# Kernel optimization log

Measured on AMD Instinct MI355X. Metric: run time of the kernel, lower is better.

## Reference

```python
import jax, jax.numpy as jnp
import numpy as np

N = 50000
E = 800000
DIM = 128          # dim_drug = atom_embedding_dim
N_ATOM_TYPES = 44
N_FIXED = 34


def setup_inputs() -> dict:
    key = jax.random.key(0)
    ks = jax.random.split(key, 9)
    x = jax.random.normal(ks[0], (N, N_ATOM_TYPES + N_FIXED), dtype=jnp.float32)
    edge_index = jax.random.randint(ks[1], (2, E), 0, N, dtype=jnp.int64)
    batch = jax.random.randint(ks[2], (N,), 0, 512, dtype=jnp.int64)
    s = 1.0 / np.sqrt(DIM)
    emb = jax.random.normal(ks[3], (N_ATOM_TYPES, DIM), dtype=jnp.float32)
    lin_W = jax.random.normal(ks[4], (DIM, DIM + N_FIXED), dtype=jnp.float32) * s
    lin_b = jnp.zeros((DIM,), dtype=jnp.float32)
    gcn1_W = jax.random.normal(ks[5], (DIM, DIM), dtype=jnp.float32) * s
    gcn1_b = jnp.zeros((DIM,), dtype=jnp.float32)
    gcn2_W = jax.random.normal(ks[6], (DIM, DIM), dtype=jnp.float32) * s
    gcn2_b = jnp.zeros((DIM,), dtype=jnp.float32)
    return {"x": x, "edge_index": edge_index, "batch": batch,
            "emb": emb, "lin_W": lin_W, "lin_b": lin_b,
            "gcn1_W": gcn1_W, "gcn1_b": gcn1_b,
            "gcn2_W": gcn2_W, "gcn2_b": gcn2_b}


def _gcn_conv(h, src, dst, norm, W, b, n):
    # PyG GCNConv: linear (no bias) -> normalized gather/scatter-add -> + bias
    h = h @ W.T                                    # [N, D]
    msg = h[src] * norm[:, None]                   # gather + scale, [E+N, D]
    out = jax.ops.segment_sum(msg, dst, num_segments=n)  # scatter-add
    return out + b


def reference(x, edge_index, batch, emb, lin_W, lin_b,
              gcn1_W, gcn1_b, gcn2_W, gcn2_b):
    n = x.shape[0]
    # embedding of argmax over one-hot atom-type block
    idx = jnp.argmax(x[:, :N_ATOM_TYPES], axis=1)
    h = jnp.concatenate([emb[idx], x[:, N_ATOM_TYPES:]], axis=1)  # [N, D+34]
    h = jax.nn.relu(h @ lin_W.T + lin_b)  # dropout = identity (eval)

    # GCN normalization with self-loops, shared by both layers
    loops = jnp.arange(n, dtype=edge_index.dtype)
    src = jnp.concatenate([edge_index[0], loops])
    dst = jnp.concatenate([edge_index[1], loops])
    deg = jax.ops.segment_sum(jnp.ones_like(dst, dtype=h.dtype), dst, num_segments=n)
    dinv = jnp.where(deg > 0, jax.lax.rsqrt(deg), 0.0)
    norm = dinv[src] * dinv[dst]                   # [E+N]

    h = jax.nn.relu(_gcn_conv(h, src, dst, norm, gcn1_W, gcn1_b, n))
    h = jax.nn.relu(_gcn_conv(h, src, dst, norm, gcn2_W, gcn2_b, n))
    return h
```

## Files before the change

### kernel.cpp

```cpp
#include <hip/hip_runtime.h>

#define NFEAT 78
#define NTYPES 44
#define NFIX 34
#define DIM 128
#define LIN_K 162
#define FIXP 36
#define APAD 132
#define TILE 32
#define RPAD 64
#define BSH 5
#define NSUB 64
#define SCAP 32

typedef unsigned int uint32;
typedef unsigned short ushort_t;

__device__ __forceinline__ uint32 ctr_decode(uint32 c) {
    uint32 p = c - 0xAAAAAAAAu;
    return (p < 1024u) ? p : c;
}

__device__ __forceinline__ unsigned short f2bf(float f) {
    uint32 u = __float_as_uint(f);
    u += 0x7FFFu + ((u >> 16) & 1u);
    return (unsigned short)(u >> 16);
}
__device__ __forceinline__ void bf_acc(uint4 v, float4& A, float4& B) {
    A.x += __uint_as_float(v.x << 16); A.y += __uint_as_float(v.x & 0xFFFF0000u);
    A.z += __uint_as_float(v.y << 16); A.w += __uint_as_float(v.y & 0xFFFF0000u);
    B.x += __uint_as_float(v.z << 16); B.y += __uint_as_float(v.z & 0xFFFF0000u);
    B.z += __uint_as_float(v.w << 16); B.w += __uint_as_float(v.w & 0xFFFF0000u);
}

__device__ __forceinline__ void agg_row(
    const ushort_t* __restrict__ row, const uint4* __restrict__ h4,
    long t, int l, int len, int NM1, float4& A, float4& B)
{
    bf_acc(h4[t * 16 + l], A, B);
    int nct = (len + 7) >> 3;
    if (nct <= 0) return;
    const uint4* row4 = (const uint4*)row;

#define MG1(D, S) { int _s = (int)(S); if (_s > NM1) _s = NM1; D = h4[(long)_s * 16 + l]; }
#define GATH8(P, I) \
    MG1(P##0, (I).x & 0xFFFFu) MG1(P##1, (I).x >> 16) \
    MG1(P##2, (I).y & 0xFFFFu) MG1(P##3, (I).y >> 16) \
    MG1(P##4, (I).z & 0xFFFFu) MG1(P##5, (I).z >> 16) \
    MG1(P##6, (I).w & 0xFFFFu) MG1(P##7, (I).w >> 16)
#define ACC8(P) \
    { bf_acc(P##0, A, B); bf_acc(P##1, A, B); bf_acc(P##2, A, B); bf_acc(P##3, A, B); \
      bf_acc(P##4, A, B); bf_acc(P##5, A, B); bf_acc(P##6, A, B); bf_acc(P##7, A, B); }
#define MACC8(P, kb) \
    { if ((kb) + 0 < len) bf_acc(P##0, A, B); \
      if ((kb) + 1 < len) bf_acc(P##1, A, B); \
      if ((kb) + 2 < len) bf_acc(P##2, A, B); \
      if ((kb) + 3 < len) bf_acc(P##3, A, B); \
      if ((kb) + 4 < len) bf_acc(P##4, A, B); \
      if ((kb) + 5 < len) bf_acc(P##5, A, B); \
      if ((kb) + 6 < len) bf_acc(P##6, A, B); \
      if ((kb) + 7 < len) bf_acc(P##7, A, B); }

    uint4 va0, va1, va2, va3, va4, va5, va6, va7;
    uint4 vb0, vb1, vb2, vb3, vb4, vb5, vb6, vb7;
    uint4 I0   = row4[0];
    uint4 Inxt = row4[1];
    GATH8(va, I0);
    int c = 1;
    for (; c + 1 < nct; c += 2) {
        uint4 Ib  = Inxt;
        uint4 In1 = row4[c + 1];
        GATH8(vb, Ib);
        int c2 = c + 2; if (c2 > 7) c2 = 7;
        uint4 In2 = row4[c2];
        ACC8(va);
        GATH8(va, In1);
        ACC8(vb);
        Inxt = In2;
    }
    if (c < nct) {
        GATH8(vb, Inxt);
        ACC8(va);
        MACC8(vb, c << 3);
    } else {
        MACC8(va, (c - 1) << 3);
    }
#undef MG1
#undef GATH8
#undef ACC8
#undef MACC8
}

__global__ __launch_bounds__(256) void k_prep(
    const int* __restrict__ esrc, const int* __restrict__ edst,
    uint32* __restrict__ bcur, uint32* __restrict__ brec, int E, int nbE, int NB,
    const float* __restrict__ w0, const float* __restrict__ w1,
    const float* __restrict__ w2, const float* __restrict__ emb,
    const float* __restrict__ lin_b,
    float* __restrict__ t0, float* __restrict__ t1, float* __restrict__ t2,
    float* __restrict__ embWb)
{
    __shared__ float smem[32 * 33];
    const int bid = blockIdx.x;
    const int tid = threadIdx.x;
    if (bid < nbE) {
        int e = bid * 256 + tid;
        if (e < E) {
            int d = edst[e], s = esrc[e];
            int sb = (bid & 63) * NB + (d >> BSH);
            uint32 old = atomicAdd(&bcur[sb], 1u);
            uint32 pos = ctr_decode(old);
            if (pos < SCAP)
                brec[(size_t)sb * SCAP + pos] = (uint32)s | ((uint32)(d & 31) << 16);
        }
        return;
    }
    if (bid < nbE + 72) {
        int bb = bid - nbE;
        int sel = bb / 24, b = bb % 24;
        const float* src = sel == 0 ? w0 : (sel == 1 ? w1 : w2);
        float*       dst = sel == 0 ? t0 : (sel == 1 ? t1 : t2);
        const int C = (sel == 0) ? LIN_K : DIM;
        int tc = (C + 31) / 32;
        int bx = b % tc, by = b / tc;
        if (by >= 4) return;
        float (*tile)[33] = (float(*)[33])smem;
        int ty = tid >> 5, tx = tid & 31;
        int c0 = bx * 32, r0 = by * 32;
        #pragma unroll
        for (int j = 0; j < 32; j += 8) {
            int r = r0 + ty + j, c = c0 + tx;
            tile[ty + j][tx] = (r < 128 && c < C) ? src[r * C + c] : 0.0f;
        }
        __syncthreads();
        #pragma unroll
        for (int j = 0; j < 32; j += 8) {
            int c = c0 + ty + j, r = r0 + tx;
            if (c < C) dst[c * 128 + r] = tile[tx][ty + j];
        }
        return;
    }
    int t = bid - nbE - 72;
    if (tid < DIM) smem[tid] = emb[t * DIM + tid];
    __syncthreads();
    if (tid < DIM) {
        float acc = lin_b[tid];
        const float* wr = w0 + (long)tid * LIN_K;
        #pragma unroll 4
        for (int k = 0; k < DIM; ++k)
            acc = fmaf(smem[k], wr[k], acc);
        embWb[t * DIM + tid] = acc;
    }
}

__global__ __launch_bounds__(256) void k_binembed(
    const uint32* __restrict__ bcur, const uint32* __restrict__ brec,
    uint32* __restrict__ cursor, ushort_t* __restrict__ csr,
    const float* __restrict__ x, const float* __restrict__ embWb,
    const float* __restrict__ W2t, const float* __restrict__ Wt,
    unsigned short* __restrict__ hs1, int N, int NB)
{
    __shared__ ushort_t lcsr[32][RPAD];
    __shared__ uint32   lcnt[32];
    __shared__ uint32   scnt[NSUB];
    __shared__ float    s_x[TILE][80];
    __shared__ int      s_idx[TILE];
    __shared__ float    s_h[TILE][APAD];
    const int b     = blockIdx.x;
    const int tid   = threadIdx.x;
    const int node0 = b * 32;

    if (tid < 32) lcnt[tid] = 0;
    if (tid < NSUB) {
        uint32 c = ctr_decode(bcur[(size_t)tid * NB + b]);
        scnt[tid] = (c < SCAP) ? c : SCAP;
    }
    {
        uint32* p = (uint32*)lcsr;
        for (int i = tid; i < 32 * RPAD / 2; i += 256) p[i] = 0xAAAAAAAAu;
    }
    __syncthreads();
    {
        const int sub = tid >> 2, r0 = tid & 3;
        uint32 cnt = scnt[sub];
        const uint32* rec = brec + ((size_t)sub * NB + b) * SCAP;
        for (uint32 r = r0; r < cnt; r += 4) {
            uint32 v = rec[r];
            int dloc = (int)(v >> 16);
            uint32 pos = atomicAdd(&lcnt[dloc], 1u);
            if (pos < RPAD) lcsr[dloc][pos] = (ushort_t)(v & 0xFFFFu);
        }
    }
    {
        const float* xb = x + (size_t)node0 * NFEAT;
        int nv = N - node0; if (nv > TILE) nv = TILE;
        int limit = nv * NFEAT;
        int nf4 = limit >> 2;
        for (int f4 = tid; f4 < nf4; f4 += 256) {
            float4 v = *(const float4*)(xb + 4 * f4);
            int f = 4 * f4;
            { int m = f / NFEAT, c = f - m * NFEAT;                s_x[m][c] = v.x; }
            { int g = f + 1; int m = g / NFEAT, c = g - m * NFEAT; s_x[m][c] = v.y; }
            { int g = f + 2; int m = g / NFEAT, c = g - m * NFEAT; s_x[m][c] = v.z; }
            { int g = f + 3; int m = g / NFEAT, c = g - m * NFEAT; s_x[m][c] = v.w; }
        }
        for (int f = (nf4 << 2) + tid; f < limit; f += 256) {
            int m = f / NFEAT, c = f - m * NFEAT;
            s_x[m][c] = xb[f];
        }
        if (nv < TILE) {
            for (int q = tid; q < (TILE - nv) * NFEAT; q += 256) {
                int m = nv + q / NFEAT, c = q % NFEAT;
                s_x[m][c] = 0.0f;
            }
        }
    }
    __syncthreads();
    {
        const uint4* src = (const uint4*)lcsr;
        uint4* dst = (uint4*)(csr + (size_t)node0 * RPAD);
        int row = tid >> 3;
        if (node0 + row < N) dst[tid] = src[tid];
        if (tid < 32 && node0 + tid < N) cursor[node0 + tid] = lcnt[tid];
    }
    if (tid < TILE) {
        int bi = 0;
        if (node0 + tid < N) {
            float best = s_x[tid][0];
            for (int k = 1; k < NTYPES; ++k) {
                float v = s_x[tid][k];
                if (v > best) { best = v; bi = k; }
            }
        }
        s_idx[tid] = bi;
    }
    __syncthreads();

    const int tx = tid & 31;
    const int m0 = (tid >> 5) * 4;
    const float4* W2t4 = (const float4*)W2t;
    const float4* eb4  = (const float4*)embWb;
    float4 acc[4];
    #pragma unroll
    for (int j = 0; j < 4; ++j) acc[j] = eb4[s_idx[m0 + j] * 32 + tx];
    for (int k = 0; k < 32; k += 8) {
        float4 w[8];
        #pragma unroll
        for (int u = 0; u < 8; ++u) w[u] = W2t4[(k + u) * 32 + tx];
        #pragma unroll
        for (int u = 0; u < 8; ++u) {
            #pragma unroll
            for (int j = 0; j < 4; ++j) {
                float a = s_x[m0 + j][NTYPES + k + u];
                acc[j].x = fmaf(a, w[u].x, acc[j].x);
                acc[j].y = fmaf(a, w[u].y, acc[j].y);
                acc[j].z = fmaf(a, w[u].z, acc[j].z);
                acc[j].w = fmaf(a, w[u].w, acc[j].w);
            }
        }
    }
    {
        float4 w0 = W2t4[32 * 32 + tx];
        float4 w1 = W2t4[33 * 32 + tx];
        #pragma unroll
        for (int j = 0; j < 4; ++j) {
            float a0 = s_x[m0 + j][NTYPES + 32], a1 = s_x[m0 + j][NTYPES + 33];
            acc[j].x = fmaf(a1, w1.x, fmaf(a0, w0.x, acc[j].x));
            acc[j].y = fmaf(a1, w1.y, fmaf(a0, w0.y, acc[j].y));
            acc[j].z = fmaf(a1, w1.z, fmaf(a0, w0.z, acc[j].z));
            acc[j].w = fmaf(a1, w1.w, fmaf(a0, w0.w, acc[j].w));
        }
    }
    #pragma unroll
    for (int j = 0; j < 4; ++j) {
        float4 o;
        o.x = fmaxf(acc[j].x, 0.0f); o.y = fmaxf(acc[j].y, 0.0f);
        o.z = fmaxf(acc[j].z, 0.0f); o.w = fmaxf(acc[j].w, 0.0f);
        *((float4*)&s_h[m0 + j][4 * tx]) = o;
    }
    __syncthreads();

    const float4* Wt4 = (const float4*)Wt;
    float4 c[4];
    #pragma unroll
    for (int j = 0; j < 4; ++j) c[j] = make_float4(0, 0, 0, 0);
    for (int k = 0; k < DIM; k += 8) {
        float4 w[8];
        #pragma unroll
        for (int u = 0; u < 8; ++u) w[u] = Wt4[(k + u) * 32 + tx];
        #pragma unroll
        for (int u = 0; u < 8; ++u) {
            #pragma unroll
            for (int j = 0; j < 4; ++j) {
                float a = s_h[m0 + j][k + u];
                c[j].x = fmaf(a, w[u].x, c[j].x);
                c[j].y = fmaf(a, w[u].y, c[j].y);
                c[j].z = fmaf(a, w[u].z, c[j].z);
                c[j].w = fmaf(a, w[u].w, c[j].w);
            }
        }
    }
    #pragma unroll
    for (int j = 0; j < 4; ++j) {
        int n = node0 + m0 + j;
        if (n < N) {
            float di = rsqrtf((float)(lcnt[m0 + j] + 1u));
            ushort4 o;
            o.x = f2bf(c[j].x * di); o.y = f2bf(c[j].y * di);
            o.z = f2bf(c[j].z * di); o.w = f2bf(c[j].w * di);
            ((ushort4*)hs1)[(long)n * 32 + tx] = o;
        }
    }
}

__global__ __launch_bounds__(256) void k_agg_gemm2(
    const ushort_t* __restrict__ csr, const uint32* __restrict__ cursor,
    const unsigned short* __restrict__ hs1, const float* __restrict__ b1,
    const float* __restrict__ Wt, unsigned short* __restrict__ hs2, int N)
{
    __shared__ float s_a[TILE][APAD];
    const int tid = threadIdx.x;
    const int node0 = blockIdx.x * TILE;
    const int qw = tid >> 4, l = tid & 15;
    const uint4* h4 = (const uint4*)hs1;
    const float4* b4 = (const float4*)b1;
    float4 bb0 = b4[2 * l], bb1 = b4[2 * l + 1];

    #pragma unroll
    for (int p = 0; p < 2; ++p) {
        int m = qw * 2 + p;
        int t = node0 + m;
        float4 A = make_float4(0, 0, 0, 0), B = make_float4(0, 0, 0, 0);
        if (t < N) {
            uint32 deg = ctr_decode(cursor[t]);
            int len = (deg < RPAD) ? (int)deg : RPAD;
            agg_row(csr + (size_t)t * RPAD, h4, (long)t, l, len, N - 1, A, B);
            float dt = rsqrtf((float)(deg + 1u));
            A.x = fmaxf(fmaf(A.x, dt, bb0.x), 0.0f);
            A.y = fmaxf(fmaf(A.y, dt, bb0.y), 0.0f);
            A.z = fmaxf(fmaf(A.z, dt, bb0.z), 0.0f);
            A.w = fmaxf(fmaf(A.w, dt, bb0.w), 0.0f);
            B.x = fmaxf(fmaf(B.x, dt, bb1.x), 0.0f);
            B.y = fmaxf(fmaf(B.y, dt, bb1.y), 0.0f);
            B.z = fmaxf(fmaf(B.z, dt, bb1.z), 0.0f);
            B.w = fmaxf(fmaf(B.w, dt, bb1.w), 0.0f);
        }
        *((float4*)&s_a[m][8 * l])     = A;
        *((float4*)&s_a[m][8 * l + 4]) = B;
    }
    __syncthreads();

    const int tx = tid & 31;
    const int m0 = (tid >> 5) * 4;
    const float4* Wt4 = (const float4*)Wt;
    float4 c[4];
    #pragma unroll
    for (int j = 0; j < 4; ++j) c[j] = make_float4(0, 0, 0, 0);
    for (int k = 0; k < DIM; k += 8) {
        float4 w[8];
        #pragma unroll
        for (int u = 0; u < 8; ++u) w[u] = Wt4[(k + u) * 32 + tx];
        #pragma unroll
        for (int u = 0; u < 8; ++u) {
            #pragma unroll
            for (int j = 0; j < 4; ++j) {
                float a = s_a[m0 + j][k + u];
                c[j].x = fmaf(a, w[u].x, c[j].x);
                c[j].y = fmaf(a, w[u].y, c[j].y);
                c[j].z = fmaf(a, w[u].z, c[j].z);
                c[j].w = fmaf(a, w[u].w, c[j].w);
            }
        }
    }
    #pragma unroll
    for (int j = 0; j < 4; ++j) {
        int n = node0 + m0 + j;
        if (n < N) {
            float di = rsqrtf((float)(ctr_decode(cursor[n]) + 1u));
            ushort4 o;
            o.x = f2bf(c[j].x * di); o.y = f2bf(c[j].y * di);
            o.z = f2bf(c[j].z * di); o.w = f2bf(c[j].w * di);
            ((ushort4*)hs2)[(long)n * 32 + tx] = o;
        }
    }
}

__global__ __launch_bounds__(256) void k_agg_out(
    const ushort_t* __restrict__ csr, const uint32* __restrict__ cursor,
    const unsigned short* __restrict__ hs2, const float* __restrict__ b2,
    float* __restrict__ out, int N)
{
    int t = blockIdx.x * 16 + (threadIdx.x >> 4);
    int l = threadIdx.x & 15;
    if (t >= N) return;
    const uint4* h4 = (const uint4*)hs2;
    const float4* b4 = (const float4*)b2;
    float4 bb0 = b4[2 * l], bb1 = b4[2 * l + 1];
    float4 A = make_float4(0, 0, 0, 0), B = make_float4(0, 0, 0, 0);
    uint32 deg = ctr_decode(cursor[t]);
    int len = (deg < RPAD) ? (int)deg : RPAD;
    agg_row(csr + (size_t)t * RPAD, h4, (long)t, l, len, N - 1, A, B);
    float dt = rsqrtf((float)(deg + 1u));
    float4 o0, o1;
    o0.x = fmaxf(fmaf(A.x, dt, bb0.x), 0.0f);
    o0.y = fmaxf(fmaf(A.y, dt, bb0.y), 0.0f);
    o0.z = fmaxf(fmaf(A.z, dt, bb0.z), 0.0f);
    o0.w = fmaxf(fmaf(A.w, dt, bb0.w), 0.0f);
    o1.x = fmaxf(fmaf(B.x, dt, bb1.x), 0.0f);
    o1.y = fmaxf(fmaf(B.y, dt, bb1.y), 0.0f);
    o1.z = fmaxf(fmaf(B.z, dt, bb1.z), 0.0f);
    o1.w = fmaxf(fmaf(B.w, dt, bb1.w), 0.0f);
    ((float4*)out)[(long)t * 32 + 2 * l]     = o0;
    ((float4*)out)[(long)t * 32 + 2 * l + 1] = o1;
}

extern "C" void kernel_launch(void* const* d_in, const int* in_sizes, int n_in,
                              void* d_out, int out_size, void* d_ws, size_t ws_size,
                              hipStream_t stream) {
    const float* x     = (const float*)d_in[0];
    const int*   edge  = (const int*)d_in[1];
    const float* emb   = (const float*)d_in[3];
    const float* lin_W = (const float*)d_in[4];
    const float* lin_b = (const float*)d_in[5];
    const float* g1W   = (const float*)d_in[6];
    const float* g1b   = (const float*)d_in[7];
    const float* g2W   = (const float*)d_in[8];
    const float* g2b   = (const float*)d_in[9];
    float* out = (float*)d_out;

    const int N = in_sizes[0] / NFEAT;
    const int E = in_sizes[1] / 2;
    const int* esrc = edge;
    const int* edst = edge + E;
    const int NB = (N + 31) / 32;

    uint32* cursor = (uint32*)d_ws;
    ushort_t* csr  = (ushort_t*)(cursor + N);
    uint32* bcur   = (uint32*)(csr + (size_t)N * RPAD);
    uint32* brec   = bcur + (size_t)NB * NSUB;
    float* linWt   = (float*)(brec + (size_t)NB * NSUB * SCAP);
    float* g1Wt    = linWt + LIN_K * DIM;
    float* g2Wt    = g1Wt + DIM * DIM;
    float* embWb   = g2Wt + DIM * DIM;
    unsigned short* hs1 = (unsigned short*)(embWb + NTYPES * DIM);
    unsigned short* hs2 = hs1 + (size_t)N * DIM;

    const int nbE  = (E + 255) / 256;
    const int nb32 = (N + TILE - 1) / TILE;
    const int nbC  = (N + 15) / 16;

    k_prep<<<nbE + 72 + NTYPES, 256, 0, stream>>>(
        esrc, edst, bcur, brec, E, nbE, NB,
        lin_W, g1W, g2W, emb, lin_b, linWt, g1Wt, g2Wt, embWb);
    k_binembed<<<NB, 256, 0, stream>>>(
        bcur, brec, cursor, csr, x, embWb, linWt + DIM * DIM, g1Wt, hs1, N, NB);
    k_agg_gemm2<<<nb32, 256, 0, stream>>>(csr, cursor, hs1, g1b, g2Wt, hs2, N);
    k_agg_out<<<nbC, 256, 0, stream>>>(csr, cursor, hs2, g2b, out, N);
}
```

Baseline: 261.4 us.

## Use split-bf16 MFMA for both GCN weight GEMMs

Replaces the scalar FP32 FMA loops for the two 128x128 GCN weight multiplies with MFMA 16x16x32 bf16 instructions. Each operand is split into hi and lo bf16 parts, and three MFMAs per tile keep accuracy close to FP32. The weights are pre-split and pre-swizzled into MFMA fragment layout in the prep kernel, and the per-row degree normalisation is cached in shared memory. The cost is extra conversion work on activations and lower-precision arithmetic, and the output stores become scattered 2-byte writes.

```diff
diff --git a/kernel.cpp b/kernel.cpp
--- a/kernel.cpp
+++ b/kernel.cpp
@@ -5,7 +5,6 @@
 #define NFIX 34
 #define DIM 128
 #define LIN_K 162
-#define FIXP 36
 #define APAD 132
 #define TILE 32
 #define RPAD 64
@@ -15,6 +14,8 @@
 
 typedef unsigned int uint32;
 typedef unsigned short ushort_t;
+typedef __attribute__((ext_vector_type(8))) short bf16x8;
+typedef __attribute__((ext_vector_type(4))) float f32x4;
 
 __device__ __forceinline__ uint32 ctr_decode(uint32 c) {
     uint32 p = c - 0xAAAAAAAAu;
@@ -25,12 +26,61 @@
     uint32 u = __float_as_uint(f);
     u += 0x7FFFu + ((u >> 16) & 1u);
     return (unsigned short)(u >> 16);
+}
+__device__ __forceinline__ float bf2f(unsigned short h) {
+    return __uint_as_float(((uint32)h) << 16);
 }
 __device__ __forceinline__ void bf_acc(uint4 v, float4& A, float4& B) {
     A.x += __uint_as_float(v.x << 16); A.y += __uint_as_float(v.x & 0xFFFF0000u);
     A.z += __uint_as_float(v.y << 16); A.w += __uint_as_float(v.y & 0xFFFF0000u);
     B.x += __uint_as_float(v.z << 16); B.y += __uint_as_float(v.z & 0xFFFF0000u);
     B.z += __uint_as_float(v.w << 16); B.w += __uint_as_float(v.w & 0xFFFF0000u);
+}
+
+__device__ __forceinline__ void mfma_gemm_store(
+    const float (*S)[APAD], const ushort_t* __restrict__ whi,
+    const ushort_t* __restrict__ wlo, const float* __restrict__ s_di,
+    unsigned short* __restrict__ hs, int node0, int N, int tid)
+{
+    const int w = tid >> 6, l = tid & 63;
+    const int rt = w & 1, cbase = (w >> 1) * 4;
+    const int lr = l & 15, lk = l >> 4;
+    const int arow = rt * 16 + lr;
+    f32x4 acc[4];
+    #pragma unroll
+    for (int c = 0; c < 4; ++c) acc[c] = (f32x4){0.f, 0.f, 0.f, 0.f};
+    const bf16x8* WH = (const bf16x8*)whi;
+    const bf16x8* WL = (const bf16x8*)wlo;
+    #pragma unroll
+    for (int K0 = 0; K0 < 4; ++K0) {
+        const float* ap = &S[arow][K0 * 32 + lk * 8];
+        bf16x8 ah, al;
+        #pragma unroll
+        for (int j = 0; j < 8; ++j) {
+            float v = ap[j];
+            unsigned short h = f2bf(v);
+            ah[j] = (short)h;
+            al[j] = (short)f2bf(v - bf2f(h));
+        }
+        #pragma unroll
+        for (int c = 0; c < 4; ++c) {
+            int f = (K0 * 8 + cbase + c) * 64 + l;
+            bf16x8 bh = WH[f], bl = WL[f];
+            acc[c] = __builtin_amdgcn_mfma_f32_16x16x32_bf16(ah, bh, acc[c], 0, 0, 0);
+            acc[c] = __builtin_amdgcn_mfma_f32_16x16x32_bf16(ah, bl, acc[c], 0, 0, 0);
+            acc[c] = __builtin_amdgcn_mfma_f32_16x16x32_bf16(al, bh, acc[c], 0, 0, 0);
+        }
+    }
+    #pragma unroll
+    for (int c = 0; c < 4; ++c) {
+        int d = (cbase + c) * 16 + lr;
+        #pragma unroll
+        for (int reg = 0; reg < 4; ++reg) {
+            int m = rt * 16 + lk * 4 + reg;
+            int n = node0 + m;
+            if (n < N) hs[(size_t)n * 128 + d] = f2bf(acc[c][reg] * s_di[m]);
+        }
+    }
 }
 
 __device__ __forceinline__ void agg_row(
@@ -97,7 +147,9 @@
     const float* __restrict__ w0, const float* __restrict__ w1,
     const float* __restrict__ w2, const float* __restrict__ emb,
     const float* __restrict__ lin_b,
-    float* __restrict__ t0, float* __restrict__ t1, float* __restrict__ t2,
+    float* __restrict__ t0,
+    ushort_t* __restrict__ g1hi, ushort_t* __restrict__ g1lo,
+    ushort_t* __restrict__ g2hi, ushort_t* __restrict__ g2lo,
     float* __restrict__ embWb)
 {
     __shared__ float smem[32 * 33];
@@ -115,12 +167,9 @@
         }
         return;
     }
-    if (bid < nbE + 72) {
-        int bb = bid - nbE;
-        int sel = bb / 24, b = bb % 24;
-        const float* src = sel == 0 ? w0 : (sel == 1 ? w1 : w2);
-        float*       dst = sel == 0 ? t0 : (sel == 1 ? t1 : t2);
-        const int C = (sel == 0) ? LIN_K : DIM;
+    if (bid < nbE + 24) {
+        int b = bid - nbE;
+        const int C = LIN_K;
         int tc = (C + 31) / 32;
         int bx = b % tc, by = b / tc;
         if (by >= 4) return;
@@ -130,17 +179,37 @@
         #pragma unroll
         for (int j = 0; j < 32; j += 8) {
             int r = r0 + ty + j, c = c0 + tx;
-            tile[ty + j][tx] = (r < 128 && c < C) ? src[r * C + c] : 0.0f;
+            tile[ty + j][tx] = (r < 128 && c < C) ? w0[r * C + c] : 0.0f;
         }
         __syncthreads();
         #pragma unroll
         for (int j = 0; j < 32; j += 8) {
             int c = c0 + ty + j, r = r0 + tx;
-            if (c < C) dst[c * 128 + r] = tile[tx][ty + j];
+            if (c < C) t0[c * 128 + r] = tile[tx][ty + j];
         }
         return;
     }
-    int t = bid - nbE - 72;
+    if (bid < nbE + 40) {
+        int bb2 = bid - nbE - 24;
+        const float* src = (bb2 >> 3) ? w2 : w1;
+        ushort_t* dhi = (bb2 >> 3) ? g2hi : g1hi;
+        ushort_t* dlo = (bb2 >> 3) ? g2lo : g1lo;
+        int base = (bb2 & 7) * 256 + tid;
+        int l = base & 63, ct = (base >> 6) & 7, K0 = base >> 9;
+        int k = K0 * 32 + (l >> 4) * 8;
+        int d = ct * 16 + (l & 15);
+        const float* sp = src + d * 128 + k;
+        size_t o = (size_t)base * 8;
+        #pragma unroll
+        for (int j = 0; j < 8; ++j) {
+            float v = sp[j];
+            unsigned short h = f2bf(v);
+            dhi[o + j] = h;
+            dlo[o + j] = f2bf(v - bf2f(h));
+        }
+        return;
+    }
+    int t = bid - nbE - 40;
     if (tid < DIM) smem[tid] = emb[t * DIM + tid];
     __syncthreads();
     if (tid < DIM) {
@@ -157,7 +226,8 @@
     const uint32* __restrict__ bcur, const uint32* __restrict__ brec,
     uint32* __restrict__ cursor, ushort_t* __restrict__ csr,
     const float* __restrict__ x, const float* __restrict__ embWb,
-    const float* __restrict__ W2t, const float* __restrict__ Wt,
+    const float* __restrict__ W2t,
+    const ushort_t* __restrict__ whi, const ushort_t* __restrict__ wlo,
     unsigned short* __restrict__ hs1, int N, int NB)
 {
     __shared__ ushort_t lcsr[32][RPAD];
@@ -166,6 +236,7 @@
     __shared__ float    s_x[TILE][80];
     __shared__ int      s_idx[TILE];
     __shared__ float    s_h[TILE][APAD];
+    __shared__ float    s_di[TILE];
     const int b     = blockIdx.x;
     const int tid   = threadIdx.x;
     const int node0 = b * 32;
@@ -222,6 +293,7 @@
         int row = tid >> 3;
         if (node0 + row < N) dst[tid] = src[tid];
         if (tid < 32 && node0 + tid < N) cursor[node0 + tid] = lcnt[tid];
+        if (tid < 32) s_di[tid] = rsqrtf((float)(lcnt[tid] + 1u));
     }
     if (tid < TILE) {
         int bi = 0;
@@ -280,45 +352,17 @@
     }
     __syncthreads();
 
-    const float4* Wt4 = (const float4*)Wt;
-    float4 c[4];
-    #pragma unroll
-    for (int j = 0; j < 4; ++j) c[j] = make_float4(0, 0, 0, 0);
-    for (int k = 0; k < DIM; k += 8) {
-        float4 w[8];
-        #pragma unroll
-        for (int u = 0; u < 8; ++u) w[u] = Wt4[(k + u) * 32 + tx];
-        #pragma unroll
-        for (int u = 0; u < 8; ++u) {
-            #pragma unroll
-            for (int j = 0; j < 4; ++j) {
-                float a = s_h[m0 + j][k + u];
-                c[j].x = fmaf(a, w[u].x, c[j].x);
-                c[j].y = fmaf(a, w[u].y, c[j].y);
-                c[j].z = fmaf(a, w[u].z, c[j].z);
-                c[j].w = fmaf(a, w[u].w, c[j].w);
-            }
-        }
-    }
-    #pragma unroll
-    for (int j = 0; j < 4; ++j) {
-        int n = node0 + m0 + j;
-        if (n < N) {
-            float di = rsqrtf((float)(lcnt[m0 + j] + 1u));
-            ushort4 o;
-            o.x = f2bf(c[j].x * di); o.y = f2bf(c[j].y * di);
-            o.z = f2bf(c[j].z * di); o.w = f2bf(c[j].w * di);
-            ((ushort4*)hs1)[(long)n * 32 + tx] = o;
-        }
-    }
+    mfma_gemm_store(s_h, whi, wlo, s_di, hs1, node0, N, tid);
 }
 
 __global__ __launch_bounds__(256) void k_agg_gemm2(
     const ushort_t* __restrict__ csr, const uint32* __restrict__ cursor,
     const unsigned short* __restrict__ hs1, const float* __restrict__ b1,
-    const float* __restrict__ Wt, unsigned short* __restrict__ hs2, int N)
+    const ushort_t* __restrict__ whi, const ushort_t* __restrict__ wlo,
+    unsigned short* __restrict__ hs2, int N)
 {
     __shared__ float s_a[TILE][APAD];
+    __shared__ float s_di[TILE];
     const int tid = threadIdx.x;
     const int node0 = blockIdx.x * TILE;
     const int qw = tid >> 4, l = tid & 15;
@@ -344,45 +388,14 @@
             B.y = fmaxf(fmaf(B.y, dt, bb1.y), 0.0f);
             B.z = fmaxf(fmaf(B.z, dt, bb1.z), 0.0f);
             B.w = fmaxf(fmaf(B.w, dt, bb1.w), 0.0f);
+            if (l == 0) s_di[m] = dt;
         }
         *((float4*)&s_a[m][8 * l])     = A;
         *((float4*)&s_a[m][8 * l + 4]) = B;
     }
     __syncthreads();
 
-    const int tx = tid & 31;
-    const int m0 = (tid >> 5) * 4;
-    const float4* Wt4 = (const float4*)Wt;
-    float4 c[4];
-    #pragma unroll
-    for (int j = 0; j < 4; ++j) c[j] = make_float4(0, 0, 0, 0);
-    for (int k = 0; k < DIM; k += 8) {
-        float4 w[8];
-        #pragma unroll
-        for (int u = 0; u < 8; ++u) w[u] = Wt4[(k + u) * 32 + tx];
-        #pragma unroll
-        for (int u = 0; u < 8; ++u) {
-            #pragma unroll
-            for (int j = 0; j < 4; ++j) {
-                float a = s_a[m0 + j][k + u];
-                c[j].x = fmaf(a, w[u].x, c[j].x);
-                c[j].y = fmaf(a, w[u].y, c[j].y);
-                c[j].z = fmaf(a, w[u].z, c[j].z);
-                c[j].w = fmaf(a, w[u].w, c[j].w);
-            }
-        }
-    }
-    #pragma unroll
-    for (int j = 0; j < 4; ++j) {
-        int n = node0 + m0 + j;
-        if (n < N) {
-            float di = rsqrtf((float)(ctr_decode(cursor[n]) + 1u));
-            ushort4 o;
-            o.x = f2bf(c[j].x * di); o.y = f2bf(c[j].y * di);
-            o.z = f2bf(c[j].z * di); o.w = f2bf(c[j].w * di);
-            ((ushort4*)hs2)[(long)n * 32 + tx] = o;
-        }
-    }
+    mfma_gemm_store(s_a, whi, wlo, s_di, hs2, node0, N, tid);
 }
 
 __global__ __launch_bounds__(256) void k_agg_out(
@@ -439,9 +452,11 @@
     uint32* bcur   = (uint32*)(csr + (size_t)N * RPAD);
     uint32* brec   = bcur + (size_t)NB * NSUB;
     float* linWt   = (float*)(brec + (size_t)NB * NSUB * SCAP);
-    float* g1Wt    = linWt + LIN_K * DIM;
-    float* g2Wt    = g1Wt + DIM * DIM;
-    float* embWb   = g2Wt + DIM * DIM;
+    ushort_t* g1hi = (ushort_t*)(linWt + LIN_K * DIM);
+    ushort_t* g1lo = g1hi + DIM * DIM;
+    ushort_t* g2hi = g1lo + DIM * DIM;
+    ushort_t* g2lo = g2hi + DIM * DIM;
+    float* embWb   = (float*)(g2lo + DIM * DIM);
     unsigned short* hs1 = (unsigned short*)(embWb + NTYPES * DIM);
     unsigned short* hs2 = hs1 + (size_t)N * DIM;
 
@@ -449,11 +464,11 @@
     const int nb32 = (N + TILE - 1) / TILE;
     const int nbC  = (N + 15) / 16;
 
-    k_prep<<<nbE + 72 + NTYPES, 256, 0, stream>>>(
+    k_prep<<<nbE + 40 + NTYPES, 256, 0, stream>>>(
         esrc, edst, bcur, brec, E, nbE, NB,
-        lin_W, g1W, g2W, emb, lin_b, linWt, g1Wt, g2Wt, embWb);
+        lin_W, g1W, g2W, emb, lin_b, linWt, g1hi, g1lo, g2hi, g2lo, embWb);
     k_binembed<<<NB, 256, 0, stream>>>(
-        bcur, brec, cursor, csr, x, embWb, linWt + DIM * DIM, g1Wt, hs1, N, NB);
-    k_agg_gemm2<<<nb32, 256, 0, stream>>>(csr, cursor, hs1, g1b, g2Wt, hs2, N);
+        bcur, brec, cursor, csr, x, embWb, linWt + DIM * DIM, g1hi, g1lo, hs1, N, NB);
+    k_agg_gemm2<<<nb32, 256, 0, stream>>>(csr, cursor, hs1, g1b, g2hi, g2lo, hs2, N);
     k_agg_out<<<nbC, 256, 0, stream>>>(csr, cursor, hs2, g2b, out, N);
 }
```

New measurement: 230.6 us. 1.13x faster.
